# Kernel tuning notes

Hardware: AMD Instinct MI355X
Metric: run time of the kernel (lower is better)

Reference implementation:

```python
import jax, jax.numpy as jnp
import numpy as np

B, S, D = 1, 2048, 2048
NH, NKV = 32, 8
HD = D // NH  # 64
ROPE_THETA = 10000.0


def setup_inputs() -> dict:
    key = jax.random.key(0)
    k1, k2, k3 = jax.random.split(key, 3)
    x = jax.random.normal(k1, (B, S, D), dtype=jnp.float32)
    # real RoPE frequencies (freqs_cis = exp(i * t * theta^(-2j/hd)))
    inv_freq = 1.0 / (ROPE_THETA ** (np.arange(0, HD, 2, dtype=np.float32) / HD))
    t = np.arange(S, dtype=np.float32)
    ang = np.outer(t, inv_freq)  # [S, HD/2]
    cos = jnp.asarray(np.cos(ang), dtype=jnp.float32)
    sin = jnp.asarray(np.sin(ang), dtype=jnp.float32)
    wqkv = jax.random.normal(k2, (NH * HD + 2 * NKV * HD, D), dtype=jnp.float32) * (D ** -0.5)
    wo = jax.random.normal(k3, (D, NH * HD), dtype=jnp.float32) * (D ** -0.5)
    return {"x": x, "cos": cos, "sin": sin, "wqkv": wqkv, "wo": wo}


def _rope(t, cos, sin):
    # t: [b, h, s, hd]; pairs are interleaved (even=real, odd=imag)
    tr = t[..., 0::2]
    ti = t[..., 1::2]
    c = cos[None, None]  # [1,1,s,hd/2]
    s_ = sin[None, None]
    orr = tr * c - ti * s_
    oi = tr * s_ + ti * c
    out = jnp.stack([orr, oi], axis=-1)  # [b,h,s,hd/2,2]
    return out.reshape(t.shape)


def reference(x, cos, sin, wqkv, wo):
    bsz, seqlen, d_model = x.shape
    qkv = jnp.einsum('bsd,ed->bse', x, wqkv)  # fused QKV proj
    q, k, v = jnp.split(qkv, [NH * HD, NH * HD + NKV * HD], axis=-1)
    q = q.reshape(bsz, seqlen, NH, HD).transpose(0, 2, 1, 3)
    k = k.reshape(bsz, seqlen, NKV, HD).transpose(0, 2, 1, 3)
    v = v.reshape(bsz, seqlen, NKV, HD).transpose(0, 2, 1, 3)
    q = _rope(q, cos, sin)
    k = _rope(k, cos, sin)
    # GQA: repeat_interleave kv heads
    rep = NH // NKV
    k_r = jnp.broadcast_to(k[:, :, None], (bsz, NKV, rep, seqlen, HD)).reshape(bsz, NH, seqlen, HD)
    v_r = jnp.broadcast_to(v[:, :, None], (bsz, NKV, rep, seqlen, HD)).reshape(bsz, NH, seqlen, HD)
    scale = 1.0 / jnp.sqrt(jnp.asarray(HD, dtype=x.dtype))
    scores = jnp.einsum('bhqd,bhkd->bhqk', q, k_r) * scale
    causal = jnp.tril(jnp.ones((seqlen, seqlen), dtype=bool))
    scores = jnp.where(causal[None, None], scores, jnp.asarray(-jnp.inf, dtype=scores.dtype))
    attn = jax.nn.softmax(scores, axis=-1)
    y = jnp.einsum('bhqk,bhkd->bhqd', attn, v_r)
    y = y.transpose(0, 2, 1, 3).reshape(bsz, seqlen, NH * HD)
    y = jnp.einsum('bse,de->bsd', y, wo)
    return y
```

## Files before the change

### kernel.cpp

```cpp
#include <hip/hip_runtime.h>
#include <hip/hip_bf16.h>

typedef __attribute__((ext_vector_type(8))) short bf16x8;
typedef __attribute__((ext_vector_type(4))) float f32x4;
typedef __attribute__((ext_vector_type(16))) float f32x16;
typedef __attribute__((ext_vector_type(2))) unsigned int u32x2;

#define S_LEN 2048
#define DMODEL 2048
#define NHEAD 32
#define NKVH 8
#define HDIM 64
#define EQKV 3072

#if defined(__has_builtin)
#if __has_builtin(__builtin_amdgcn_global_load_lds)
#define HAVE_GLL 1
#endif
#endif

__device__ __forceinline__ unsigned short f2bf(float f) {
  unsigned int u = __float_as_uint(f);
  u = (u + 0x7FFFu + ((u >> 16) & 1u)) >> 16;
  return (unsigned short)u;
}

__device__ __forceinline__ f32x4 mfma16(bf16x8 a, bf16x8 b, f32x4 c) {
  return __builtin_amdgcn_mfma_f32_16x16x32_bf16(a, b, c, 0, 0, 0);
}
__device__ __forceinline__ f32x16 mfma32(bf16x8 a, bf16x8 b, f32x16 c) {
  return __builtin_amdgcn_mfma_f32_32x32x16_bf16(a, b, c, 0, 0, 0);
}

__device__ __forceinline__ unsigned cvtpk(float a, float b) {
  unsigned r;
  asm("v_cvt_pk_bf16_f32 %0, %1, %2" : "=v"(r) : "v"(a), "v"(b));
  return r;
}

__device__ __forceinline__ void plswap(unsigned& a, unsigned& b) {
  u32x2 r = __builtin_amdgcn_permlane32_swap(a, b, false, false);
  a = r.x;
  b = r.y;
}
__device__ __forceinline__ void plswapf(float& a, float& b) {
  unsigned ua = __float_as_uint(a), ub = __float_as_uint(b);
  plswap(ua, ub);
  a = __uint_as_float(ua);
  b = __uint_as_float(ub);
}

#if HAVE_GLL
__device__ __forceinline__ void gload16(const unsigned short* g,
                                        unsigned short* l) {
  __builtin_amdgcn_global_load_lds(
      (const __attribute__((address_space(1))) unsigned int*)g,
      (__attribute__((address_space(3))) unsigned int*)l, 16, 0, 0);
}
#endif

__global__ void cast3_kernel(const float* __restrict__ x,
                             const float* __restrict__ wqkv,
                             const float* __restrict__ wo,
                             unsigned short* __restrict__ xb,
                             unsigned short* __restrict__ wb,
                             unsigned short* __restrict__ wob) {
  int i = blockIdx.x * blockDim.x + threadIdx.x;
  const float* s;
  unsigned short* d;
  int j;
  if (i < 1048576) {
    s = x; d = xb; j = i;
  } else if (i < 2621440) {
    s = wqkv; d = wb; j = i - 1048576;
  } else {
    s = wo; d = wob; j = i - 2621440;
  }
  float4 v = ((const float4*)s)[j];
  ushort4 o;
  o.x = f2bf(v.x); o.y = f2bf(v.y); o.z = f2bf(v.z); o.w = f2bf(v.w);
  ((ushort4*)d)[j] = o;
}

__launch_bounds__(256)
__global__ void gemm_bt(const unsigned short* __restrict__ A,
                        const unsigned short* __restrict__ B,
                        float* __restrict__ C, int M, int N, int K) {
  __shared__ unsigned short As[2][128 * 64];
  __shared__ unsigned short Bs[2][64 * 64];
  const int tid = threadIdx.x;
  const int w = tid >> 6, l = tid & 63;
  const int wr = w >> 1, wc = w & 1;
  const int nwg = gridDim.x * gridDim.y;
  const int bid0 = blockIdx.y * gridDim.x + blockIdx.x;
  const int swz = (bid0 & 7) * (nwg >> 3) + (bid0 >> 3);
  const int bm = swz / gridDim.x, bn = swz % gridDim.x;
  const int lr = l & 15, lq = l >> 4;

  f32x4 acc[4][2];
#pragma unroll
  for (int m = 0; m < 4; ++m)
#pragma unroll
    for (int n = 0; n < 2; ++n) acc[m][n] = (f32x4)0.f;

  const unsigned short* gA[4];
  const unsigned short* gB[2];
#pragma unroll
  for (int i = 0; i < 4; ++i) {
    int c = i * 256 + tid;
    int row = c >> 3;
    int sc = (c & 7) ^ (row & 7);
    gA[i] = A + (size_t)(bm * 128 + row) * K + sc * 8;
  }
#pragma unroll
  for (int i = 0; i < 2; ++i) {
    int c = i * 256 + tid;
    int row = c >> 3;
    int sc = (c & 7) ^ (row & 7);
    gB[i] = B + (size_t)(bn * 64 + row) * K + sc * 8;
  }

#if HAVE_GLL
#define STAGE(bufi, k0)                                            \
  do {                                                             \
    _Pragma("unroll") for (int i = 0; i < 4; ++i)                  \
        gload16(gA[i] + (k0), &As[bufi][(i * 256 + w * 64) * 8]);  \
    _Pragma("unroll") for (int i = 0; i < 2; ++i)                  \
        gload16(gB[i] + (k0), &Bs[bufi][(i * 256 + w * 64) * 8]);  \
  } while (0)
#else
#define STAGE(bufi, k0)                                            \
  do {                                                             \
    _Pragma("unroll") for (int i = 0; i < 4; ++i) {                \
      int c = i * 256 + tid;                                       \
      *(uint4*)(&As[bufi][c * 8]) = *(const uint4*)(gA[i] + (k0)); \
    }                                                              \
    _Pragma("unroll") for (int i = 0; i < 2; ++i) {                \
      int c = i * 256 + tid;                                       \
      *(uint4*)(&Bs[bufi][c * 8]) = *(const uint4*)(gB[i] + (k0)); \
    }                                                              \
  } while (0)
#endif

#define COMPUTE(bufi)                                                     \
  do {                                                                    \
    _Pragma("unroll") for (int ks = 0; ks < 2; ++ks) {                    \
      bf16x8 af[4], bfr[2];                                               \
      _Pragma("unroll") for (int m = 0; m < 4; ++m) {                     \
        int row = wr * 64 + m * 16 + lr;                                  \
        int ch = (ks * 4 + lq) ^ (row & 7);                               \
        af[m] = *(const bf16x8*)(&As[bufi][row * 64 + ch * 8]);           \
      }                                                                   \
      _Pragma("unroll") for (int n = 0; n < 2; ++n) {                     \
        int row = wc * 32 + n * 16 + lr;                                  \
        int ch = (ks * 4 + lq) ^ (row & 7);                               \
        bfr[n] = *(const bf16x8*)(&Bs[bufi][row * 64 + ch * 8]);          \
      }                                                                   \
      _Pragma("unroll") for (int m = 0; m < 4; ++m)                       \
          _Pragma("unroll") for (int n = 0; n < 2; ++n)                   \
              acc[m][n] = mfma16(af[m], bfr[n], acc[m][n]);               \
    }                                                                     \
  } while (0)

  const int nt = K >> 6;
  STAGE(0, 0);
  int cur = 0;
#if HAVE_GLL
  for (int t = 0; t < nt - 1; ++t) {
    STAGE(cur ^ 1, (t + 1) * 64);
    asm volatile("s_waitcnt vmcnt(6)" ::: "memory");
    __builtin_amdgcn_sched_barrier(0);
    __builtin_amdgcn_s_barrier();
    COMPUTE(cur);
    asm volatile("s_waitcnt lgkmcnt(0)" ::: "memory");
    __builtin_amdgcn_sched_barrier(0);
    __builtin_amdgcn_s_barrier();
    cur ^= 1;
  }
  asm volatile("s_waitcnt vmcnt(0)" ::: "memory");
  __builtin_amdgcn_sched_barrier(0);
  __builtin_amdgcn_s_barrier();
  COMPUTE(cur);
#else
  for (int t = 0; t < nt; ++t) {
    if (t > 0) STAGE(cur, t * 64);
    __syncthreads();
    COMPUTE(cur);
    __syncthreads();
  }
#endif
#undef STAGE
#undef COMPUTE

  const int r0 = bm * 128 + wr * 64;
  const int c0 = bn * 64 + wc * 32;
#pragma unroll
  for (int m = 0; m < 4; ++m)
#pragma unroll
    for (int n = 0; n < 2; ++n)
#pragma unroll
      for (int r = 0; r < 4; ++r)
        C[(size_t)(r0 + m * 16 + 4 * lq + r) * N + c0 + n * 16 + lr] =
            acc[m][n][r];
}

#define KSCALE 0.18033688011112042f
__global__ void rope_split(const float* __restrict__ qkv,
                           const float* __restrict__ cosb,
                           const float* __restrict__ sinb,
                           unsigned short* __restrict__ qb,
                           unsigned short* __restrict__ kft) {
  const int s = blockIdx.x;
  const float* row = qkv + (size_t)s * EQKV;
  for (int idx = threadIdx.x; idx < 1280; idx += 256) {
    int hh = idx >> 5;
    int m = idx & 31;
    float c = cosb[s * 32 + m];
    float sn = sinb[s * 32 + m];
    if (hh < 32) {
      float tr = row[hh * 64 + 2 * m];
      float ti = row[hh * 64 + 2 * m + 1];
      unsigned int pack = (unsigned int)f2bf(tr * c - ti * sn) |
                          ((unsigned int)f2bf(tr * sn + ti * c) << 16);
      *(unsigned int*)(qb + ((size_t)hh * S_LEN + s) * HDIM + 2 * m) = pack;
    } else {
      int kvh = hh - 32;
      float cs = c * KSCALE, ss = sn * KSCALE;
      float tr = row[2048 + kvh * 64 + 2 * m];
      float ti = row[2048 + kvh * 64 + 2 * m + 1];
      unsigned int pack = (unsigned int)f2bf(tr * cs - ti * ss) |
                          ((unsigned int)f2bf(tr * ss + ti * cs) << 16);
      int kt = s >> 5, lq = s & 31;
      int j = m >> 3, hi = (m >> 2) & 1;
      unsigned short* dst =
          kft +
          ((((size_t)kvh * 64 + kt) * 4 + j) * 64 + lq + 32 * hi) * 8 +
          (m & 3) * 2;
      *(unsigned int*)dst = pack;
    }
  }
}

__global__ void v_transpose(const float* __restrict__ qkv,
                            unsigned short* __restrict__ vft) {
  __shared__ unsigned short tile[64][72];
  const int kvh = blockIdx.x;
  const int st = blockIdx.y;
  const int t = threadIdx.x;
  {
    const int sl = t >> 2, dg = t & 3;
    const float* src =
        qkv + (size_t)(st * 64 + sl) * EQKV + 2560 + kvh * 64 + dg * 16;
#pragma unroll
    for (int j = 0; j < 16; ++j) tile[dg * 16 + j][sl] = f2bf(src[j]);
  }
  __syncthreads();
  {
    const int kt_local = t >> 7, c = (t >> 5) & 3, lq2 = t & 31;
    const int kt = st * 2 + kt_local;
    const int d = ((c >> 1) & 1) * 32 + lq2;
    unsigned short* dbase =
        vft + (((size_t)(kvh * 64 + kt) * 4 + c) * 64) * 8;
#pragma unroll
    for (int hi2 = 0; hi2 < 2; ++hi2) {
      int koff = kt_local * 32 + (c & 1) * 16 + 8 * hi2;
      *(uint4*)(dbase + (lq2 + 32 * hi2) * 8) =
          *(const uint4*)(&tile[d][koff]);
    }
  }
}

__launch_bounds__(256, 3)
__global__ void attn_kernel(const unsigned short* __restrict__ qb,
                            const unsigned short* __restrict__ kft,
                            const unsigned short* __restrict__ vft,
                            unsigned short* __restrict__ aob) {
  __shared__ float buf[4][64][19];
  const int tid = threadIdx.x;
  const int wv = tid >> 6, l = tid & 63;
  const int bid = blockIdx.x;
  const int h = bid & 31;
  const int qt = 63 - (bid >> 5);
  const int kvh = h >> 2;
  const int q0 = qt << 5;
  const int lq = l & 31;
  const int hi = l >> 5;
  const int qg = q0 + lq;

  const unsigned short* qrow = qb + ((size_t)h * S_LEN + qg) * HDIM + 8 * hi;
  bf16x8 qf[4];
#pragma unroll
  for (int j = 0; j < 4; ++j) qf[j] = *(const bf16x8*)(qrow + 16 * j);

  const unsigned short* kbase = kft + (size_t)kvh * 64 * 2048;
  const unsigned short* vbase = vft + (size_t)kvh * 64 * 2048;

  f32x16 o0 = (f32x16)0.f, o1 = (f32x16)0.f;
  float mrun = -1e30f, lrun = 0.f;
  const int ntile = qt + 1;

  int kt = wv;
  for (; kt + 4 < ntile; kt += 8) {
    const unsigned short* ka = kbase + (size_t)kt * 2048;
    const unsigned short* va = vbase + (size_t)kt * 2048;
    bf16x8 kfa[4], kfb[4], vaa[4], vab[4];
#pragma unroll
    for (int j = 0; j < 4; ++j) {
      kfa[j] = *(const bf16x8*)(ka + 512 * j + l * 8);
      kfb[j] = *(const bf16x8*)(ka + 4 * 2048 + 512 * j + l * 8);
      vaa[j] = *(const bf16x8*)(va + 512 * j + l * 8);
      vab[j] = *(const bf16x8*)(va + 4 * 2048 + 512 * j + l * 8);
    }
    f32x16 sa = (f32x16)0.f, sb = (f32x16)0.f;
    __builtin_amdgcn_s_setprio(1);
#pragma unroll
    for (int j = 0; j < 4; ++j) sa = mfma32(kfa[j], qf[j], sa);
#pragma unroll
    for (int j = 0; j < 4; ++j) sb = mfma32(kfb[j], qf[j], sb);
    __builtin_amdgcn_s_setprio(0);

    float p[32];
#pragma unroll
    for (int r = 0; r < 16; ++r) p[r] = sa[r];
    if (kt + 4 == ntile - 1) {
#pragma unroll
      for (int r = 0; r < 16; ++r) {
        int key = (kt + 4) * 32 + (r & 3) + 8 * (r >> 2) + 4 * hi;
        p[16 + r] = (key > qg) ? -1e30f : sb[r];
      }
    } else {
#pragma unroll
      for (int r = 0; r < 16; ++r) p[16 + r] = sb[r];
    }
    float a0 = fmaxf(fmaxf(p[0], p[1]), p[2]);
    float a1 = fmaxf(fmaxf(p[3], p[4]), p[5]);
    float a2 = fmaxf(fmaxf(p[6], p[7]), p[8]);
    float a3 = fmaxf(fmaxf(p[9], p[10]), p[11]);
    float a4 = fmaxf(fmaxf(p[12], p[13]), p[14]);
    float b0 = fmaxf(fmaxf(p[15], p[16]), p[17]);
    float b1 = fmaxf(fmaxf(p[18], p[19]), p[20]);
    float b2 = fmaxf(fmaxf(p[21], p[22]), p[23]);
    float b3 = fmaxf(fmaxf(p[24], p[25]), p[26]);
    float b4 = fmaxf(fmaxf(p[27], p[28]), p[29]);
    float b5 = fmaxf(p[30], p[31]);
    float mt = fmaxf(fmaxf(fmaxf(fmaxf(a0, a1), fmaxf(a2, a3)),
                           fmaxf(fmaxf(a4, b0), fmaxf(b1, b2))),
                     fmaxf(fmaxf(b3, b4), b5));
    float mto = mt;
    plswapf(mt, mto);
    mt = fmaxf(mt, mto);
    if (!__all(mt - mrun <= 8.f)) {
      float mnew = fmaxf(mrun, mt);
      float al = __builtin_amdgcn_exp2f(mrun - mnew);
      mrun = mnew;
      lrun *= al;
      o0 *= al;
      o1 *= al;
    }
#pragma unroll
    for (int r = 0; r < 32; ++r) p[r] = __builtin_amdgcn_exp2f(p[r] - mrun);
    float s0 = (p[0] + p[1]) + (p[2] + p[3]);
    float s1 = (p[4] + p[5]) + (p[6] + p[7]);
    float s2 = (p[8] + p[9]) + (p[10] + p[11]);
    float s3 = (p[12] + p[13]) + (p[14] + p[15]);
    float s4 = (p[16] + p[17]) + (p[18] + p[19]);
    float s5 = (p[20] + p[21]) + (p[22] + p[23]);
    float s6 = (p[24] + p[25]) + (p[26] + p[27]);
    float s7 = (p[28] + p[29]) + (p[30] + p[31]);
    float ts = ((s0 + s1) + (s2 + s3)) + ((s4 + s5) + (s6 + s7));
    float tso = ts;
    plswapf(ts, tso);
    ts += tso;
    lrun += ts;
    union B8 { unsigned u[4]; bf16x8 v; } pb0a, pb1a, pb0b, pb1b;
    {
      unsigned t0 = cvtpk(p[0], p[1]), t1 = cvtpk(p[4], p[5]);
      plswap(t0, t1);
      pb0a.u[0] = t0; pb0a.u[2] = t1;
    }
    {
      unsigned t0 = cvtpk(p[2], p[3]), t1 = cvtpk(p[6], p[7]);
      plswap(t0, t1);
      pb0a.u[1] = t0; pb0a.u[3] = t1;
    }
    {
      unsigned t0 = cvtpk(p[8], p[9]), t1 = cvtpk(p[12], p[13]);
      plswap(t0, t1);
      pb1a.u[0] = t0; pb1a.u[2] = t1;
    }
    {
      unsigned t0 = cvtpk(p[10], p[11]), t1 = cvtpk(p[14], p[15]);
      plswap(t0, t1);
      pb1a.u[1] = t0; pb1a.u[3] = t1;
    }
    {
      unsigned t0 = cvtpk(p[16], p[17]), t1 = cvtpk(p[20], p[21]);
      plswap(t0, t1);
      pb0b.u[0] = t0; pb0b.u[2] = t1;
    }
    {
      unsigned t0 = cvtpk(p[18], p[19]), t1 = cvtpk(p[22], p[23]);
      plswap(t0, t1);
      pb0b.u[1] = t0; pb0b.u[3] = t1;
    }
    {
      unsigned t0 = cvtpk(p[24], p[25]), t1 = cvtpk(p[28], p[29]);
      plswap(t0, t1);
      pb1b.u[0] = t0; pb1b.u[2] = t1;
    }
    {
      unsigned t0 = cvtpk(p[26], p[27]), t1 = cvtpk(p[30], p[31]);
      plswap(t0, t1);
      pb1b.u[1] = t0; pb1b.u[3] = t1;
    }
    __builtin_amdgcn_s_setprio(1);
    o0 = mfma32(vaa[0], pb0a.v, o0);
    o0 = mfma32(vaa[1], pb1a.v, o0);
    o1 = mfma32(vaa[2], pb0a.v, o1);
    o1 = mfma32(vaa[3], pb1a.v, o1);
    o0 = mfma32(vab[0], pb0b.v, o0);
    o0 = mfma32(vab[1], pb1b.v, o0);
    o1 = mfma32(vab[2], pb0b.v, o1);
    o1 = mfma32(vab[3], pb1b.v, o1);
    __builtin_amdgcn_s_setprio(0);
  }
  if (kt < ntile) {
    const int key0 = kt << 5;
    const unsigned short* kvt = kbase + (size_t)kt * 2048;
    bf16x8 kf0 = *(const bf16x8*)(kvt + l * 8);
    bf16x8 kf1 = *(const bf16x8*)(kvt + 512 + l * 8);
    bf16x8 kf2 = *(const bf16x8*)(kvt + 1024 + l * 8);
    bf16x8 kf3 = *(const bf16x8*)(kvt + 1536 + l * 8);
    const unsigned short* vvt = vbase + (size_t)kt * 2048;
    bf16x8 va00 = *(const bf16x8*)(vvt + l * 8);
    bf16x8 va01 = *(const bf16x8*)(vvt + 512 + l * 8);
    bf16x8 va10 = *(const bf16x8*)(vvt + 1024 + l * 8);
    bf16x8 va11 = *(const bf16x8*)(vvt + 1536 + l * 8);

    f32x16 s = (f32x16)0.f;
    __builtin_amdgcn_s_setprio(1);
    s = mfma32(kf0, qf[0], s);
    s = mfma32(kf1, qf[1], s);
    s = mfma32(kf2, qf[2], s);
    s = mfma32(kf3, qf[3], s);
    __builtin_amdgcn_s_setprio(0);

    float p[16];
    if (kt == ntile - 1) {
#pragma unroll
      for (int r = 0; r < 16; ++r) {
        int key = key0 + (r & 3) + 8 * (r >> 2) + 4 * hi;
        p[r] = (key > qg) ? -1e30f : s[r];
      }
    } else {
#pragma unroll
      for (int r = 0; r < 16; ++r) p[r] = s[r];
    }
    float a0 = fmaxf(fmaxf(p[0], p[1]), p[2]);
    float a1 = fmaxf(fmaxf(p[3], p[4]), p[5]);
    float a2 = fmaxf(fmaxf(p[6], p[7]), p[8]);
    float a3 = fmaxf(fmaxf(p[9], p[10]), p[11]);
    float a4 = fmaxf(fmaxf(p[12], p[13]), p[14]);
    float mt = fmaxf(fmaxf(fmaxf(a0, a1), a2), fmaxf(fmaxf(a3, a4), p[15]));
    float mto = mt;
    plswapf(mt, mto);
    mt = fmaxf(mt, mto);
    if (!__all(mt - mrun <= 8.f)) {
      float mnew = fmaxf(mrun, mt);
      float al = __builtin_amdgcn_exp2f(mrun - mnew);
      mrun = mnew;
      lrun *= al;
      o0 *= al;
      o1 *= al;
    }
#pragma unroll
    for (int r = 0; r < 16; ++r) p[r] = __builtin_amdgcn_exp2f(p[r] - mrun);
    float s0 = (p[0] + p[1]) + (p[2] + p[3]);
    float s1 = (p[4] + p[5]) + (p[6] + p[7]);
    float s2 = (p[8] + p[9]) + (p[10] + p[11]);
    float s3 = (p[12] + p[13]) + (p[14] + p[15]);
    float ts = (s0 + s1) + (s2 + s3);
    float tso = ts;
    plswapf(ts, tso);
    ts += tso;
    lrun += ts;
    union B8 { unsigned u[4]; bf16x8 v; } pb0, pb1;
    {
      unsigned t0 = cvtpk(p[0], p[1]), t1 = cvtpk(p[4], p[5]);
      plswap(t0, t1);
      pb0.u[0] = t0; pb0.u[2] = t1;
    }
    {
      unsigned t0 = cvtpk(p[2], p[3]), t1 = cvtpk(p[6], p[7]);
      plswap(t0, t1);
      pb0.u[1] = t0; pb0.u[3] = t1;
    }
    {
      unsigned t0 = cvtpk(p[8], p[9]), t1 = cvtpk(p[12], p[13]);
      plswap(t0, t1);
      pb1.u[0] = t0; pb1.u[2] = t1;
    }
    {
      unsigned t0 = cvtpk(p[10], p[11]), t1 = cvtpk(p[14], p[15]);
      plswap(t0, t1);
      pb1.u[1] = t0; pb1.u[3] = t1;
    }
    __builtin_amdgcn_s_setprio(1);
    o0 = mfma32(va00, pb0.v, o0);
    o0 = mfma32(va01, pb1.v, o0);
    o1 = mfma32(va10, pb0.v, o1);
    o1 = mfma32(va11, pb1.v, o1);
    __builtin_amdgcn_s_setprio(0);
  }

  {
    union F16 { f32x16 v; f32x4 q[4]; } uu;
    uu.v = o0;
    float* dst = &buf[wv][l][0];
#pragma unroll
    for (int i = 0; i < 4; ++i) *(f32x4*)(dst + 4 * i) = uu.q[i];
    dst[16] = mrun;
    dst[17] = lrun;
  }
  __syncthreads();
  float mfin = -1e30f;
#pragma unroll
  for (int w2 = 0; w2 < 4; ++w2) mfin = fmaxf(mfin, buf[w2][l][16]);
  float lsum = 0.f;
  float scl[4];
#pragma unroll
  for (int w2 = 0; w2 < 4; ++w2) {
    scl[w2] = __builtin_amdgcn_exp2f(buf[w2][l][16] - mfin);
    lsum += buf[w2][l][17] * scl[w2];
  }
  const float inv = 1.f / lsum;
  unsigned short* obase = aob + (size_t)qg * DMODEL + h * 64;
  {
    f32x4 acc = (f32x4)0.f;
#pragma unroll
    for (int w2 = 0; w2 < 4; ++w2)
      acc += *(const f32x4*)&buf[w2][l][wv * 4] * scl[w2];
    unsigned u0 = cvtpk(acc[0] * inv, acc[1] * inv);
    unsigned u1 = cvtpk(acc[2] * inv, acc[3] * inv);
    unsigned short* dsto = obase + 8 * wv + 4 * hi;
    *(unsigned*)(dsto) = u0;
    *(unsigned*)(dsto + 2) = u1;
  }
  __syncthreads();
  {
    union F16 { f32x16 v; f32x4 q[4]; } uu;
    uu.v = o1;
    float* dst = &buf[wv][l][0];
#pragma unroll
    for (int i = 0; i < 4; ++i) *(f32x4*)(dst + 4 * i) = uu.q[i];
  }
  __syncthreads();
  {
    f32x4 acc = (f32x4)0.f;
#pragma unroll
    for (int w2 = 0; w2 < 4; ++w2)
      acc += *(const f32x4*)&buf[w2][l][wv * 4] * scl[w2];
    unsigned u0 = cvtpk(acc[0] * inv, acc[1] * inv);
    unsigned u1 = cvtpk(acc[2] * inv, acc[3] * inv);
    unsigned short* dsto = obase + 32 + 8 * wv + 4 * hi;
    *(unsigned*)(dsto) = u0;
    *(unsigned*)(dsto + 2) = u1;
  }
}

extern "C" void kernel_launch(void* const* d_in, const int* in_sizes, int n_in,
                              void* d_out, int out_size, void* d_ws,
                              size_t ws_size, hipStream_t stream) {
  const float* x = (const float*)d_in[0];
  const float* cosb = (const float*)d_in[1];
  const float* sinb = (const float*)d_in[2];
  const float* wqkv = (const float*)d_in[3];
  const float* wo = (const float*)d_in[4];
  float* out = (float*)d_out;
  char* ws = (char*)d_ws;
  float* qkv = (float*)(ws);
  unsigned short* xb = (unsigned short*)(ws + 25165824);
  unsigned short* wb = (unsigned short*)(ws + 33554432);
  unsigned short* wob = (unsigned short*)(ws + 46137344);
  unsigned short* qb = (unsigned short*)(ws + 54525952);
  unsigned short* kft = (unsigned short*)(ws + 62914560);
  unsigned short* vft = (unsigned short*)(ws + 65011712);
  unsigned short* aob = (unsigned short*)(ws + 67108864);

  cast3_kernel<<<dim3(3670016 / 256), 256, 0, stream>>>(x, wqkv, wo, xb, wb,
                                                        wob);
  gemm_bt<<<dim3(48, 16), 256, 0, stream>>>(xb, wb, qkv, 2048, 3072, 2048);
  rope_split<<<dim3(2048), 256, 0, stream>>>(qkv, cosb, sinb, qb, kft);
  v_transpose<<<dim3(8, 32), 256, 0, stream>>>(qkv, vft);
  attn_kernel<<<dim3(2048), 256, 0, stream>>>(qb, kft, vft, aob);
  gemm_bt<<<dim3(32, 16), 256, 0, stream>>>(aob, wob, out, 2048, 2048, 2048);
}
```

Before: 121.6 us.

## Fuse rope and V transpose, emit bf16 V from GEMM, retune attention

The QKV GEMM epilogue now writes the V columns directly as bf16 into a separate buffer instead of fp32, and the rope and V-transpose kernels are merged into a single launch that reads that bf16 V. The goal is to cut one kernel launch and the fp32 V traffic. Separately, the attention kernel raises its launch-bounds occupancy hint from 3 to 4 and issues the V loads after the QK MFMAs to reduce register pressure. The higher occupancy target may force register spills.

```diff
diff --git a/kernel.cpp b/kernel.cpp
--- a/kernel.cpp
+++ b/kernel.cpp
@@ -82,10 +82,12 @@
   ((ushort4*)d)[j] = o;
 }
 
+template <int MODE>
 __launch_bounds__(256)
 __global__ void gemm_bt(const unsigned short* __restrict__ A,
                         const unsigned short* __restrict__ B,
-                        float* __restrict__ C, int M, int N, int K) {
+                        float* __restrict__ C,
+                        unsigned short* __restrict__ VB, int M, int N, int K) {
   __shared__ unsigned short As[2][128 * 64];
   __shared__ unsigned short Bs[2][64 * 64];
   const int tid = threadIdx.x;
@@ -194,83 +196,103 @@
 
   const int r0 = bm * 128 + wr * 64;
   const int c0 = bn * 64 + wc * 32;
-#pragma unroll
-  for (int m = 0; m < 4; ++m)
-#pragma unroll
-    for (int n = 0; n < 2; ++n)
-#pragma unroll
-      for (int r = 0; r < 4; ++r)
-        C[(size_t)(r0 + m * 16 + 4 * lq + r) * N + c0 + n * 16 + lr] =
-            acc[m][n][r];
+  if (MODE == 1 && bn >= 40) {
+    const int c0v = c0 - 2560;
+#pragma unroll
+    for (int m = 0; m < 4; ++m)
+#pragma unroll
+      for (int n = 0; n < 2; ++n)
+#pragma unroll
+        for (int r = 0; r < 4; ++r)
+          VB[(size_t)(r0 + m * 16 + 4 * lq + r) * 512 + c0v + n * 16 + lr] =
+              f2bf(acc[m][n][r]);
+  } else {
+#pragma unroll
+    for (int m = 0; m < 4; ++m)
+#pragma unroll
+      for (int n = 0; n < 2; ++n)
+#pragma unroll
+        for (int r = 0; r < 4; ++r)
+          C[(size_t)(r0 + m * 16 + 4 * lq + r) * N + c0 + n * 16 + lr] =
+              acc[m][n][r];
+  }
 }
 
 #define KSCALE 0.18033688011112042f
-__global__ void rope_split(const float* __restrict__ qkv,
-                           const float* __restrict__ cosb,
-                           const float* __restrict__ sinb,
-                           unsigned short* __restrict__ qb,
-                           unsigned short* __restrict__ kft) {
-  const int s = blockIdx.x;
-  const float* row = qkv + (size_t)s * EQKV;
-  for (int idx = threadIdx.x; idx < 1280; idx += 256) {
-    int hh = idx >> 5;
-    int m = idx & 31;
-    float c = cosb[s * 32 + m];
-    float sn = sinb[s * 32 + m];
-    if (hh < 32) {
-      float tr = row[hh * 64 + 2 * m];
-      float ti = row[hh * 64 + 2 * m + 1];
-      unsigned int pack = (unsigned int)f2bf(tr * c - ti * sn) |
-                          ((unsigned int)f2bf(tr * sn + ti * c) << 16);
-      *(unsigned int*)(qb + ((size_t)hh * S_LEN + s) * HDIM + 2 * m) = pack;
-    } else {
-      int kvh = hh - 32;
-      float cs = c * KSCALE, ss = sn * KSCALE;
-      float tr = row[2048 + kvh * 64 + 2 * m];
-      float ti = row[2048 + kvh * 64 + 2 * m + 1];
-      unsigned int pack = (unsigned int)f2bf(tr * cs - ti * ss) |
-                          ((unsigned int)f2bf(tr * ss + ti * cs) << 16);
-      int kt = s >> 5, lq = s & 31;
-      int j = m >> 3, hi = (m >> 2) & 1;
-      unsigned short* dst =
-          kft +
-          ((((size_t)kvh * 64 + kt) * 4 + j) * 64 + lq + 32 * hi) * 8 +
-          (m & 3) * 2;
-      *(unsigned int*)dst = pack;
-    }
-  }
-}
-
-__global__ void v_transpose(const float* __restrict__ qkv,
-                            unsigned short* __restrict__ vft) {
+__global__ void rope_vt(const float* __restrict__ qkv,
+                        const unsigned short* __restrict__ vb,
+                        const float* __restrict__ cosb,
+                        const float* __restrict__ sinb,
+                        unsigned short* __restrict__ qb,
+                        unsigned short* __restrict__ kft,
+                        unsigned short* __restrict__ vft) {
   __shared__ unsigned short tile[64][72];
-  const int kvh = blockIdx.x;
-  const int st = blockIdx.y;
-  const int t = threadIdx.x;
-  {
-    const int sl = t >> 2, dg = t & 3;
-    const float* src =
-        qkv + (size_t)(st * 64 + sl) * EQKV + 2560 + kvh * 64 + dg * 16;
-#pragma unroll
-    for (int j = 0; j < 16; ++j) tile[dg * 16 + j][sl] = f2bf(src[j]);
-  }
-  __syncthreads();
-  {
-    const int kt_local = t >> 7, c = (t >> 5) & 3, lq2 = t & 31;
-    const int kt = st * 2 + kt_local;
-    const int d = ((c >> 1) & 1) * 32 + lq2;
-    unsigned short* dbase =
-        vft + (((size_t)(kvh * 64 + kt) * 4 + c) * 64) * 8;
-#pragma unroll
-    for (int hi2 = 0; hi2 < 2; ++hi2) {
-      int koff = kt_local * 32 + (c & 1) * 16 + 8 * hi2;
-      *(uint4*)(dbase + (lq2 + 32 * hi2) * 8) =
-          *(const uint4*)(&tile[d][koff]);
-    }
-  }
-}
-
-__launch_bounds__(256, 3)
+  const int b = blockIdx.x;
+  if (b < 2048) {
+    const int s = b;
+    const float* row = qkv + (size_t)s * EQKV;
+    for (int idx = threadIdx.x; idx < 1280; idx += 256) {
+      int hh = idx >> 5;
+      int m = idx & 31;
+      float c = cosb[s * 32 + m];
+      float sn = sinb[s * 32 + m];
+      if (hh < 32) {
+        float tr = row[hh * 64 + 2 * m];
+        float ti = row[hh * 64 + 2 * m + 1];
+        unsigned int pack = (unsigned int)f2bf(tr * c - ti * sn) |
+                            ((unsigned int)f2bf(tr * sn + ti * c) << 16);
+        *(unsigned int*)(qb + ((size_t)hh * S_LEN + s) * HDIM + 2 * m) = pack;
+      } else {
+        int kvh = hh - 32;
+        float cs = c * KSCALE, ss = sn * KSCALE;
+        float tr = row[2048 + kvh * 64 + 2 * m];
+        float ti = row[2048 + kvh * 64 + 2 * m + 1];
+        unsigned int pack = (unsigned int)f2bf(tr * cs - ti * ss) |
+                            ((unsigned int)f2bf(tr * ss + ti * cs) << 16);
+        int kt = s >> 5, lq = s & 31;
+        int j = m >> 3, hi = (m >> 2) & 1;
+        unsigned short* dst =
+            kft +
+            ((((size_t)kvh * 64 + kt) * 4 + j) * 64 + lq + 32 * hi) * 8 +
+            (m & 3) * 2;
+        *(unsigned int*)dst = pack;
+      }
+    }
+  } else {
+    const int b2 = b - 2048;
+    const int kvh = b2 >> 5;
+    const int st = b2 & 31;
+    const int t = threadIdx.x;
+    {
+      const int sl = t >> 2, dg = t & 3;
+      const unsigned short* src =
+          vb + (size_t)(st * 64 + sl) * 512 + kvh * 64 + dg * 16;
+      union U8 { uint4 v; unsigned short e[8]; } a0, a1;
+      a0.v = *(const uint4*)src;
+      a1.v = *(const uint4*)(src + 8);
+#pragma unroll
+      for (int j = 0; j < 8; ++j) tile[dg * 16 + j][sl] = a0.e[j];
+#pragma unroll
+      for (int j = 0; j < 8; ++j) tile[dg * 16 + 8 + j][sl] = a1.e[j];
+    }
+    __syncthreads();
+    {
+      const int kt_local = t >> 7, c = (t >> 5) & 3, lq2 = t & 31;
+      const int kt = st * 2 + kt_local;
+      const int d = ((c >> 1) & 1) * 32 + lq2;
+      unsigned short* dbase =
+          vft + (((size_t)(kvh * 64 + kt) * 4 + c) * 64) * 8;
+#pragma unroll
+      for (int hi2 = 0; hi2 < 2; ++hi2) {
+        int koff = kt_local * 32 + (c & 1) * 16 + 8 * hi2;
+        *(uint4*)(dbase + (lq2 + 32 * hi2) * 8) =
+            *(const uint4*)(&tile[d][koff]);
+      }
+    }
+  }
+}
+
+__launch_bounds__(256, 4)
 __global__ void attn_kernel(const unsigned short* __restrict__ qb,
                             const unsigned short* __restrict__ kft,
                             const unsigned short* __restrict__ vft,
@@ -303,21 +325,25 @@
   for (; kt + 4 < ntile; kt += 8) {
     const unsigned short* ka = kbase + (size_t)kt * 2048;
     const unsigned short* va = vbase + (size_t)kt * 2048;
-    bf16x8 kfa[4], kfb[4], vaa[4], vab[4];
+    bf16x8 kfa[4], kfb[4];
 #pragma unroll
     for (int j = 0; j < 4; ++j) {
       kfa[j] = *(const bf16x8*)(ka + 512 * j + l * 8);
       kfb[j] = *(const bf16x8*)(ka + 4 * 2048 + 512 * j + l * 8);
+    }
+    f32x16 sa = (f32x16)0.f, sb = (f32x16)0.f;
+    __builtin_amdgcn_s_setprio(1);
+#pragma unroll
+    for (int j = 0; j < 4; ++j) sa = mfma32(kfa[j], qf[j], sa);
+#pragma unroll
+    for (int j = 0; j < 4; ++j) sb = mfma32(kfb[j], qf[j], sb);
+    __builtin_amdgcn_s_setprio(0);
+    bf16x8 vaa[4], vab[4];
+#pragma unroll
+    for (int j = 0; j < 4; ++j) {
       vaa[j] = *(const bf16x8*)(va + 512 * j + l * 8);
       vab[j] = *(const bf16x8*)(va + 4 * 2048 + 512 * j + l * 8);
     }
-    f32x16 sa = (f32x16)0.f, sb = (f32x16)0.f;
-    __builtin_amdgcn_s_setprio(1);
-#pragma unroll
-    for (int j = 0; j < 4; ++j) sa = mfma32(kfa[j], qf[j], sa);
-#pragma unroll
-    for (int j = 0; j < 4; ++j) sb = mfma32(kfb[j], qf[j], sb);
-    __builtin_amdgcn_s_setprio(0);
 
     float p[32];
 #pragma unroll
@@ -431,11 +457,6 @@
     bf16x8 kf1 = *(const bf16x8*)(kvt + 512 + l * 8);
     bf16x8 kf2 = *(const bf16x8*)(kvt + 1024 + l * 8);
     bf16x8 kf3 = *(const bf16x8*)(kvt + 1536 + l * 8);
-    const unsigned short* vvt = vbase + (size_t)kt * 2048;
-    bf16x8 va00 = *(const bf16x8*)(vvt + l * 8);
-    bf16x8 va01 = *(const bf16x8*)(vvt + 512 + l * 8);
-    bf16x8 va10 = *(const bf16x8*)(vvt + 1024 + l * 8);
-    bf16x8 va11 = *(const bf16x8*)(vvt + 1536 + l * 8);
 
     f32x16 s = (f32x16)0.f;
     __builtin_amdgcn_s_setprio(1);
@@ -444,6 +465,11 @@
     s = mfma32(kf2, qf[2], s);
     s = mfma32(kf3, qf[3], s);
     __builtin_amdgcn_s_setprio(0);
+    const unsigned short* vvt = vbase + (size_t)kt * 2048;
+    bf16x8 va00 = *(const bf16x8*)(vvt + l * 8);
+    bf16x8 va01 = *(const bf16x8*)(vvt + 512 + l * 8);
+    bf16x8 va10 = *(const bf16x8*)(vvt + 1024 + l * 8);
+    bf16x8 va11 = *(const bf16x8*)(vvt + 1536 + l * 8);
 
     float p[16];
     if (kt == ntile - 1) {
@@ -586,12 +612,14 @@
   unsigned short* kft = (unsigned short*)(ws + 62914560);
   unsigned short* vft = (unsigned short*)(ws + 65011712);
   unsigned short* aob = (unsigned short*)(ws + 67108864);
+  unsigned short* vb = (unsigned short*)(ws + 75497472);
 
   cast3_kernel<<<dim3(3670016 / 256), 256, 0, stream>>>(x, wqkv, wo, xb, wb,
                                                         wob);
-  gemm_bt<<<dim3(48, 16), 256, 0, stream>>>(xb, wb, qkv, 2048, 3072, 2048);
-  rope_split<<<dim3(2048), 256, 0, stream>>>(qkv, cosb, sinb, qb, kft);
-  v_transpose<<<dim3(8, 32), 256, 0, stream>>>(qkv, vft);
+  gemm_bt<1><<<dim3(48, 16), 256, 0, stream>>>(xb, wb, qkv, vb, 2048, 3072,
+                                               2048);
+  rope_vt<<<dim3(2304), 256, 0, stream>>>(qkv, vb, cosb, sinb, qb, kft, vft);
   attn_kernel<<<dim3(2048), 256, 0, stream>>>(qb, kft, vft, aob);
-  gemm_bt<<<dim3(32, 16), 256, 0, stream>>>(aob, wob, out, 2048, 2048, 2048);
-}
+  gemm_bt<0><<<dim3(32, 16), 256, 0, stream>>>(aob, wob, out, nullptr, 2048,
+                                               2048, 2048);
+}
```

Result: slower. 134.8 us (+10.9%).
